# Kernel tuning notes

Hardware: AMD Instinct MI355X
Metric: run time of the kernel (lower is better)

The kernel has to match this reference:

```python
import jax, jax.numpy as jnp
import numpy as np

D_MODEL = 1024
H = 16
D_K = D_MODEL // H

def setup_inputs() -> dict:
    key = jax.random.key(0)
    k1, k2, k3, k4, k5 = jax.random.split(key, 5)
    x = jax.random.normal(k1, (2, 2048, D_MODEL), dtype=jnp.float32)
    s = 1.0 / np.sqrt(D_MODEL)
    W_qkv = jax.random.uniform(k2, (D_MODEL, 3 * D_MODEL), jnp.float32, -s, s)
    b_qkv = jax.random.uniform(k3, (3 * D_MODEL,), jnp.float32, -s, s)
    W_o = jax.random.uniform(k4, (D_MODEL, D_MODEL), jnp.float32, -s, s)
    b_o = jax.random.uniform(k5, (D_MODEL,), jnp.float32, -s, s)
    return {"x": x, "W_qkv": W_qkv, "b_qkv": b_qkv, "W_o": W_o, "b_o": b_o}

def reference(x, W_qkv, b_qkv, W_o, b_o):
    B, L, _ = x.shape
    qkv = x @ W_qkv + b_qkv                      # [B, L, 3*d_model]
    q, k, v = jnp.split(qkv, 3, axis=-1)
    def split_heads(t):
        return t.reshape(B, L, H, D_K).transpose(0, 2, 1, 3)  # [B,H,L,D_k]
    q, k, v = split_heads(q), split_heads(k), split_heads(v)
    scores = jnp.einsum('bhqd,bhkd->bhqk', q, k) / np.sqrt(D_K).astype(jnp.float32)
    attn = jax.nn.softmax(scores, axis=-1)       # [B,H,L,L]
    ctx = jnp.einsum('bhqk,bhkd->bhqd', attn, v)
    ctx = ctx.transpose(0, 2, 1, 3).reshape(B, L, H * D_K)
    out = ctx @ W_o + b_o                        # dropout is identity at eval
    return (out, attn)
```

## Files before the change

kernel.cpp:

```cpp
#include <hip/hip_runtime.h>
#include <stdint.h>

typedef __attribute__((ext_vector_type(8))) short bf16x8;
typedef __attribute__((ext_vector_type(4))) float f32x4;
typedef __attribute__((ext_vector_type(4))) unsigned int u32x4;
typedef __attribute__((ext_vector_type(4))) unsigned short u16x4;

#define DEVINL static __device__ __forceinline__

DEVINL unsigned short f2bf(float f) {
  uint32_t u = __builtin_bit_cast(uint32_t, f);
  u = (u + 0x7FFFu + ((u >> 16) & 1u)) >> 16;
  return (unsigned short)u;
}

DEVINL float fexp2(float x) {
#if __has_builtin(__builtin_amdgcn_exp2f)
  return __builtin_amdgcn_exp2f(x);
#else
  return __expf(x * 0.69314718056f);
#endif
}

DEVINL void raw_barrier() {
  __builtin_amdgcn_sched_barrier(0);
  __builtin_amdgcn_s_barrier();
  __builtin_amdgcn_sched_barrier(0);
}

DEVINL void barrier_lds_only() {
  asm volatile("s_waitcnt lgkmcnt(0)" ::: "memory");
  raw_barrier();
}

DEVINL bf16x8 pack8(f32x4 a, f32x4 b) {
  union { uint32_t u[4]; bf16x8 v; } r;
  asm("v_cvt_pk_bf16_f32 %0, %1, %2" : "=v"(r.u[0]) : "v"(a[0]), "v"(a[1]));
  asm("v_cvt_pk_bf16_f32 %0, %1, %2" : "=v"(r.u[1]) : "v"(a[2]), "v"(a[3]));
  asm("v_cvt_pk_bf16_f32 %0, %1, %2" : "=v"(r.u[2]) : "v"(b[0]), "v"(b[1]));
  asm("v_cvt_pk_bf16_f32 %0, %1, %2" : "=v"(r.u[3]) : "v"(b[2]), "v"(b[3]));
  return r.v;
}

DEVINL void async16(const unsigned short* lds, const unsigned short* g) {
  __builtin_amdgcn_global_load_lds(
      (const __attribute__((address_space(1))) unsigned int*)g,
      (__attribute__((address_space(3))) unsigned int*)lds, 16, 0, 0);
}

__global__ __launch_bounds__(256) void k_prep(const float* __restrict__ x,
                                              unsigned short* __restrict__ xbf,
                                              const float* __restrict__ Wqkv,
                                              unsigned short* __restrict__ wqT,
                                              const float* __restrict__ Wo,
                                              unsigned short* __restrict__ woT) {
  int bid = blockIdx.x;
  int t = threadIdx.x;
  if (bid < 4096) {
    int i = bid * 256 + t;
    f32x4 v = *(const f32x4*)(x + (size_t)i * 4);
    u16x4 o;
    for (int j = 0; j < 4; ++j) o[j] = f2bf(v[j]);
    *(u16x4*)(xbf + (size_t)i * 4) = o;
    return;
  }
  __shared__ unsigned short tile[64][72];
  const float* in;
  unsigned short* out;
  int K = 1024, N, k0, n0;
  if (bid < 4864) {
    int b = bid - 4096;
    N = 3072; k0 = (b & 15) * 64; n0 = (b >> 4) * 64;
    in = Wqkv; out = wqT;
  } else {
    int b = bid - 4864;
    N = 1024; k0 = (b & 15) * 64; n0 = (b >> 4) * 64;
    in = Wo; out = woT;
  }
  int r = t >> 2, c0 = (t & 3) * 16;
  for (int j = 0; j < 4; ++j) {
    int col = c0 + j * 4;
    f32x4 v = *(const f32x4*)(in + (size_t)(k0 + r) * N + n0 + col);
    u16x4 o;
    for (int q = 0; q < 4; ++q) o[q] = f2bf(v[q]);
    *(u16x4*)(&tile[r][col]) = o;
  }
  __syncthreads();
  for (int j = 0; j < 4; ++j) {
    int kcol = c0 + j * 4;
    u16x4 o;
    for (int q = 0; q < 4; ++q) o[q] = tile[kcol + q][r];
    *(u16x4*)(out + (size_t)(n0 + r) * K + k0 + kcol) = o;
  }
}

template <int MODE>
__global__ __launch_bounds__(256) void k_gemm(const unsigned short* __restrict__ A,
                                              const unsigned short* __restrict__ Bt,
                                              const float* __restrict__ bias,
                                              unsigned short* __restrict__ Qb,
                                              unsigned short* __restrict__ Kb,
                                              unsigned short* __restrict__ Vt,
                                              float* __restrict__ outF) {
  constexpr int KD = 1024;
  __shared__ unsigned short sh[17408];
  unsigned short* lA = sh;
  unsigned short* lB = sh + 8192;
  int tid = threadIdx.x;
  int lane = tid & 63, w = tid >> 6;
  int wr = w >> 1, wc = w & 1;
  int m0 = blockIdx.x * 128, n0 = blockIdx.y * 128;
  int lr = lane & 15, lg = lane >> 4;

  f32x4 acc[4][4] = {};

  int srow = w * 32 + (lane >> 3);
  int scol = (lane & 7) * 8;
  const unsigned short* gA = A + (size_t)(m0 + srow) * KD + scol;
  const unsigned short* gB = Bt + (size_t)(n0 + srow) * KD + scol;

  for (int kk = 0; kk < KD; kk += 64) {
    for (int s = 0; s < 4; ++s) {
      async16(&lA[(w * 32 + s * 8) * 64], gA + (size_t)s * 8 * KD + kk);
      async16(&lB[(w * 32 + s * 8) * 64], gB + (size_t)s * 8 * KD + kk);
    }
    __syncthreads();
    for (int kq = 0; kq < 2; ++kq) {
      bf16x8 af[4], bfr[4];
      for (int i = 0; i < 4; ++i)
        af[i] = *(const bf16x8*)(&lA[(wr * 64 + i * 16 + lr) * 64 + (kq * 4 + lg) * 8]);
      for (int r = 0; r < 4; ++r)
        bfr[r] = *(const bf16x8*)(&lB[(wc * 64 + r * 16 + lr) * 64 + (kq * 4 + lg) * 8]);
      for (int i = 0; i < 4; ++i)
        for (int r = 0; r < 4; ++r)
          acc[i][r] = __builtin_amdgcn_mfma_f32_16x16x32_bf16(af[i], bfr[r], acc[i][r], 0, 0, 0);
    }
    __syncthreads();
  }

  if (MODE == 0) {
    int which = n0 >> 10;
    int head0 = (n0 & 1023) >> 6;
    int b_idx = m0 >> 11;
    int l0 = m0 & 2047;
    if (which < 2) {
      for (int r = 0; r < 4; ++r) {
        int nl = wc * 64 + r * 16 + lr;
        float bv = bias[n0 + nl];
        for (int i = 0; i < 4; ++i) {
          int mlb = wr * 64 + i * 16 + lg * 4;
          for (int jj = 0; jj < 4; ++jj)
            sh[(mlb + jj) * 136 + nl] = f2bf(acc[i][r][jj] + bv);
        }
      }
      __syncthreads();
      unsigned short* dst = (which == 0) ? Qb : Kb;
      for (int it = 0; it < 4; ++it) {
        int row = it * 64 + (tid >> 2);
        int ml = row & 127, hd = row >> 7;
        int c = (tid & 3) * 16;
        bf16x8 v0 = *(const bf16x8*)&sh[ml * 136 + hd * 64 + c];
        bf16x8 v1 = *(const bf16x8*)&sh[ml * 136 + hd * 64 + c + 8];
        size_t bh = (size_t)(b_idx * 16 + head0 + hd);
        size_t off = (bh * 2048 + l0 + ml) * 64 + c;
        *(bf16x8*)(dst + off) = v0;
        *(bf16x8*)(dst + off + 8) = v1;
      }
    } else {
      for (int r = 0; r < 4; ++r) {
        int nl = wc * 64 + r * 16 + lr;
        float bv = bias[n0 + nl];
        for (int i = 0; i < 4; ++i) {
          int mlb = wr * 64 + i * 16 + lg * 4;
          u16x4 pk;
          for (int jj = 0; jj < 4; ++jj) pk[jj] = f2bf(acc[i][r][jj] + bv);
          *(u16x4*)&sh[nl * 136 + mlb] = pk;
        }
      }
      __syncthreads();
      for (int it = 0; it < 4; ++it) {
        int nl = it * 32 + (tid >> 3);
        int c = (tid & 7) * 16;
        bf16x8 v0 = *(const bf16x8*)&sh[nl * 136 + c];
        bf16x8 v1 = *(const bf16x8*)&sh[nl * 136 + c + 8];
        int dk = nl & 63, hd = nl >> 6;
        size_t bh = (size_t)(b_idx * 16 + head0 + hd);
        size_t off = (bh * 64 + dk) * 2048 + l0 + c;
        *(bf16x8*)(Vt + off) = v0;
        *(bf16x8*)(Vt + off + 8) = v1;
      }
    }
  } else {
    for (int r = 0; r < 4; ++r) {
      int n = n0 + wc * 64 + r * 16 + lr;
      float bv = bias[n];
      for (int i = 0; i < 4; ++i) {
        int mb = m0 + wr * 64 + i * 16 + lg * 4;
        for (int jj = 0; jj < 4; ++jj)
          outF[(size_t)(mb + jj) * 1024 + n] = acc[i][r][jj] + bv;
      }
    }
  }
}

__global__ __launch_bounds__(256) void k_attn(const unsigned short* __restrict__ Qb,
                                              const unsigned short* __restrict__ Kb,
                                              const unsigned short* __restrict__ Vt,
                                              float* __restrict__ attn,
                                              unsigned short* __restrict__ ctx) {
  __shared__ unsigned short Ks[2][4096];
  __shared__ unsigned short Vs[2][4096];
  __shared__ float Pf[4][32 * 68];
  int tid = threadIdx.x, lane = tid & 63, w = tid >> 6;
  int lr = lane & 15, lg = lane >> 4;
  int bid = blockIdx.x;
  int xcd = bid & 7, slot = bid >> 3;
  int bh = xcd * 4 + (slot >> 4);
  int qb = slot & 15;
  int q0 = qb * 128 + w * 32;
  int b_idx = bh >> 4, h = bh & 15;
  const unsigned short* Qh = Qb + (size_t)bh * 2048 * 64;
  const unsigned short* Kh = Kb + (size_t)bh * 2048 * 64;
  const unsigned short* Vh = Vt + (size_t)bh * 64 * 2048;
  float* Pw = &Pf[w][0];
  const float A2 = 0.125f * 1.44269504089f;
  int e7 = lr & 7;

  int srow = w * 8 + (lane >> 3);
  int sc = (lane & 7) ^ (srow & 7);
  const unsigned short* gK = Kh + (size_t)srow * 64 + sc * 8;
  const unsigned short* gV = Vh + (size_t)srow * 2048 + sc * 8;

  bf16x8 qf[2][2];
  for (int i = 0; i < 2; ++i)
    for (int kq = 0; kq < 2; ++kq)
      qf[i][kq] = *(const bf16x8*)(Qh + (size_t)(q0 + i * 16 + lr) * 64 + kq * 32 + lg * 8);

  float l_run[2] = {0.f, 0.f};

  async16(&Ks[0][(w * 8) * 64],       gK);
  async16(&Ks[0][((w + 4) * 8) * 64], gK + 2048);
  for (int kt = 0; kt < 32; ++kt) {
    int cur = kt & 1;
    if (kt < 31) {
      async16(&Ks[cur ^ 1][(w * 8) * 64],       gK + (size_t)(kt + 1) * 4096);
      async16(&Ks[cur ^ 1][((w + 4) * 8) * 64], gK + (size_t)(kt + 1) * 4096 + 2048);
      asm volatile("s_waitcnt vmcnt(2)" ::: "memory");
    } else {
      asm volatile("s_waitcnt vmcnt(0)" ::: "memory");
    }
    raw_barrier();
    f32x4 acc[2][4] = {};
    for (int kq = 0; kq < 2; ++kq) {
      int j = kq * 4 + lg;
      bf16x8 kf[4];
      for (int r = 0; r < 4; ++r)
        kf[r] = *(const bf16x8*)&Ks[cur][(r * 16 + lr) * 64 + ((j ^ e7) << 3)];
      for (int i = 0; i < 2; ++i)
        for (int r = 0; r < 4; ++r)
          acc[i][r] = __builtin_amdgcn_mfma_f32_16x16x32_bf16(kf[r], qf[i][kq], acc[i][r], 0, 0, 0);
    }
    for (int i = 0; i < 2; ++i)
      for (int r = 0; r < 4; ++r)
        l_run[i] += fexp2(acc[i][r][0] * A2) + fexp2(acc[i][r][1] * A2) +
                    fexp2(acc[i][r][2] * A2) + fexp2(acc[i][r][3] * A2);
    barrier_lds_only();
  }
  float invl[2];
  for (int i = 0; i < 2; ++i) {
    float s = l_run[i];
    s += __shfl_xor(s, 16);
    s += __shfl_xor(s, 32);
    invl[i] = 1.0f / s;
  }

  f32x4 cacc[2][4] = {};
  float* attn_base = attn + (size_t)bh * 2048 * 2048;
  float* arow = attn_base + (size_t)(q0 + lg) * 2048 + lr * 4;

  async16(&Ks[0][(w * 8) * 64],       gK);
  async16(&Ks[0][((w + 4) * 8) * 64], gK + 2048);
  async16(&Vs[0][(w * 8) * 64],       gV);
  async16(&Vs[0][((w + 4) * 8) * 64], gV + 65536);
  for (int kt = 0; kt < 32; ++kt) {
    int cur = kt & 1;
    if (kt < 31) {
      async16(&Ks[cur ^ 1][(w * 8) * 64],       gK + (size_t)(kt + 1) * 4096);
      async16(&Ks[cur ^ 1][((w + 4) * 8) * 64], gK + (size_t)(kt + 1) * 4096 + 2048);
      async16(&Vs[cur ^ 1][(w * 8) * 64],       gV + (size_t)(kt + 1) * 64);
      async16(&Vs[cur ^ 1][((w + 4) * 8) * 64], gV + (size_t)(kt + 1) * 64 + 65536);
    }
    if (kt == 0)       asm volatile("s_waitcnt vmcnt(4)" ::: "memory");
    else if (kt == 31) asm volatile("s_waitcnt vmcnt(8)" ::: "memory");
    else               asm volatile("s_waitcnt vmcnt(12)" ::: "memory");
    raw_barrier();
    f32x4 acc[2][4] = {};
    for (int kq = 0; kq < 2; ++kq) {
      int j = kq * 4 + lg;
      bf16x8 kf[4];
      for (int r = 0; r < 4; ++r)
        kf[r] = *(const bf16x8*)&Ks[cur][(r * 16 + lr) * 64 + ((j ^ e7) << 3)];
      for (int i = 0; i < 2; ++i)
        for (int r = 0; r < 4; ++r)
          acc[i][r] = __builtin_amdgcn_mfma_f32_16x16x32_bf16(kf[r], qf[i][kq], acc[i][r], 0, 0, 0);
    }
    for (int i = 0; i < 2; ++i)
      for (int r = 0; r < 4; ++r) {
        f32x4 pv;
        for (int jj = 0; jj < 4; ++jj)
          pv[jj] = fexp2(acc[i][r][jj] * A2) * invl[i];
        *(f32x4*)&Pw[(i * 16 + lr) * 68 + r * 16 + lg * 4] = pv;
      }
    for (int s = 0; s < 8; ++s) {
      f32x4 v = *(const f32x4*)(&Pw[(s * 4 + lg) * 68 + lr * 4]);
      __builtin_nontemporal_store(v, (f32x4*)(arow + (size_t)s * 4 * 2048 + kt * 64));
    }
    for (int kq2 = 0; kq2 < 2; ++kq2) {
      int j = kq2 * 4 + lg;
      int kof = kq2 * 32 + lg * 8;
      bf16x8 pa[2], vf[4];
      for (int i = 0; i < 2; ++i) {
        f32x4 plo = *(const f32x4*)(&Pw[(i * 16 + lr) * 68 + kof]);
        f32x4 phi = *(const f32x4*)(&Pw[(i * 16 + lr) * 68 + kof + 4]);
        pa[i] = pack8(plo, phi);
      }
      for (int nn = 0; nn < 4; ++nn)
        vf[nn] = *(const bf16x8*)&Vs[cur][(nn * 16 + lr) * 64 + ((j ^ e7) << 3)];
      for (int i = 0; i < 2; ++i)
        for (int nn = 0; nn < 4; ++nn)
          cacc[i][nn] = __builtin_amdgcn_mfma_f32_16x16x32_bf16(pa[i], vf[nn], cacc[i][nn], 0, 0, 0);
    }
    barrier_lds_only();
  }

  for (int nn = 0; nn < 4; ++nn) {
    int d = nn * 16 + lr;
    for (int i = 0; i < 2; ++i)
      for (int jj = 0; jj < 4; ++jj) {
        int q = q0 + i * 16 + lg * 4 + jj;
        int tok = b_idx * 2048 + q;
        ctx[(size_t)tok * 1024 + h * 64 + d] = f2bf(cacc[i][nn][jj]);
      }
  }
}

extern "C" void kernel_launch(void* const* d_in, const int* in_sizes, int n_in,
                              void* d_out, int out_size, void* d_ws, size_t ws_size,
                              hipStream_t stream) {
  const float* x    = (const float*)d_in[0];
  const float* Wqkv = (const float*)d_in[1];
  const float* bqkv = (const float*)d_in[2];
  const float* Wo   = (const float*)d_in[3];
  const float* bo   = (const float*)d_in[4];
  float* out  = (float*)d_out;
  float* attn = out + (size_t)4096 * 1024;

  char* ws = (char*)d_ws;
  unsigned short* xbf = (unsigned short*)(ws);
  unsigned short* wqT = (unsigned short*)(ws + 8388608);
  unsigned short* woT = (unsigned short*)(ws + 14680064);
  unsigned short* Qb  = (unsigned short*)(ws + 16777216);
  unsigned short* Kb  = (unsigned short*)(ws + 25165824);
  unsigned short* Vt  = (unsigned short*)(ws + 33554432);
  unsigned short* ctx = (unsigned short*)(ws + 41943040);

  k_prep<<<dim3(5120), dim3(256), 0, stream>>>(x, xbf, Wqkv, wqT, Wo, woT);
  k_gemm<0><<<dim3(32, 24), dim3(256), 0, stream>>>(xbf, wqT, bqkv, Qb, Kb, Vt, nullptr);
  k_attn<<<dim3(512), dim3(256), 0, stream>>>(Qb, Kb, Vt, attn, ctx);
  k_gemm<1><<<dim3(32, 8), dim3(256), 0, stream>>>(ctx, woT, bo, nullptr, nullptr, nullptr, out);
}
```

Measured before the change: 232.9 us.

## Stage softmax probabilities as bf16 in LDS and deepen K prefetch ring

The attention kernel now converts probabilities to packed bf16 once and keeps them in a bf16 LDS buffer. That buffer feeds the PV MFMA directly and is widened back to fp32 for the attn output store, which halves the P staging footprint and removes the fp32 re-read and repack. K and V buffers are merged into one 4-slot LDS array. The first (row-sum) pass uses a prefetch distance of two with the per-iteration trailing barrier removed. The returned attention matrix is now rounded to bf16 precision, which adds output error, and the lower LDS use may allow higher occupancy.

```diff
diff --git a/kernel.cpp b/kernel.cpp
--- a/kernel.cpp
+++ b/kernel.cpp
@@ -4,6 +4,7 @@
 typedef __attribute__((ext_vector_type(8))) short bf16x8;
 typedef __attribute__((ext_vector_type(4))) float f32x4;
 typedef __attribute__((ext_vector_type(4))) unsigned int u32x4;
+typedef __attribute__((ext_vector_type(2))) unsigned int u32x2;
 typedef __attribute__((ext_vector_type(4))) unsigned short u16x4;
 
 #define DEVINL static __device__ __forceinline__
@@ -31,15 +32,6 @@
 DEVINL void barrier_lds_only() {
   asm volatile("s_waitcnt lgkmcnt(0)" ::: "memory");
   raw_barrier();
-}
-
-DEVINL bf16x8 pack8(f32x4 a, f32x4 b) {
-  union { uint32_t u[4]; bf16x8 v; } r;
-  asm("v_cvt_pk_bf16_f32 %0, %1, %2" : "=v"(r.u[0]) : "v"(a[0]), "v"(a[1]));
-  asm("v_cvt_pk_bf16_f32 %0, %1, %2" : "=v"(r.u[1]) : "v"(a[2]), "v"(a[3]));
-  asm("v_cvt_pk_bf16_f32 %0, %1, %2" : "=v"(r.u[2]) : "v"(b[0]), "v"(b[1]));
-  asm("v_cvt_pk_bf16_f32 %0, %1, %2" : "=v"(r.u[3]) : "v"(b[2]), "v"(b[3]));
-  return r.v;
 }
 
 DEVINL void async16(const unsigned short* lds, const unsigned short* g) {
@@ -208,9 +200,8 @@
                                               const unsigned short* __restrict__ Vt,
                                               float* __restrict__ attn,
                                               unsigned short* __restrict__ ctx) {
-  __shared__ unsigned short Ks[2][4096];
-  __shared__ unsigned short Vs[2][4096];
-  __shared__ float Pf[4][32 * 68];
+  __shared__ unsigned short KVs[4][4096];
+  __shared__ uint32_t Pb[4][32 * 36];
   int tid = threadIdx.x, lane = tid & 63, w = tid >> 6;
   int lr = lane & 15, lg = lane >> 4;
   int bid = blockIdx.x;
@@ -222,7 +213,7 @@
   const unsigned short* Qh = Qb + (size_t)bh * 2048 * 64;
   const unsigned short* Kh = Kb + (size_t)bh * 2048 * 64;
   const unsigned short* Vh = Vt + (size_t)bh * 64 * 2048;
-  float* Pw = &Pf[w][0];
+  uint32_t* PwB = &Pb[w][0];
   const float A2 = 0.125f * 1.44269504089f;
   int e7 = lr & 7;
 
@@ -238,13 +229,17 @@
 
   float l_run[2] = {0.f, 0.f};
 
-  async16(&Ks[0][(w * 8) * 64],       gK);
-  async16(&Ks[0][((w + 4) * 8) * 64], gK + 2048);
+  async16(&KVs[0][(w * 8) * 64],       gK);
+  async16(&KVs[0][((w + 4) * 8) * 64], gK + 2048);
+  async16(&KVs[1][(w * 8) * 64],       gK + 4096);
+  async16(&KVs[1][((w + 4) * 8) * 64], gK + 4096 + 2048);
   for (int kt = 0; kt < 32; ++kt) {
-    int cur = kt & 1;
-    if (kt < 31) {
-      async16(&Ks[cur ^ 1][(w * 8) * 64],       gK + (size_t)(kt + 1) * 4096);
-      async16(&Ks[cur ^ 1][((w + 4) * 8) * 64], gK + (size_t)(kt + 1) * 4096 + 2048);
+    const unsigned short* Kc = KVs[kt & 3];
+    if (kt < 30) {
+      async16(&KVs[(kt + 2) & 3][(w * 8) * 64],       gK + (size_t)(kt + 2) * 4096);
+      async16(&KVs[(kt + 2) & 3][((w + 4) * 8) * 64], gK + (size_t)(kt + 2) * 4096 + 2048);
+      asm volatile("s_waitcnt vmcnt(4)" ::: "memory");
+    } else if (kt == 30) {
       asm volatile("s_waitcnt vmcnt(2)" ::: "memory");
     } else {
       asm volatile("s_waitcnt vmcnt(0)" ::: "memory");
@@ -255,7 +250,7 @@
       int j = kq * 4 + lg;
       bf16x8 kf[4];
       for (int r = 0; r < 4; ++r)
-        kf[r] = *(const bf16x8*)&Ks[cur][(r * 16 + lr) * 64 + ((j ^ e7) << 3)];
+        kf[r] = *(const bf16x8*)&Kc[(r * 16 + lr) * 64 + ((j ^ e7) << 3)];
       for (int i = 0; i < 2; ++i)
         for (int r = 0; r < 4; ++r)
           acc[i][r] = __builtin_amdgcn_mfma_f32_16x16x32_bf16(kf[r], qf[i][kq], acc[i][r], 0, 0, 0);
@@ -264,7 +259,6 @@
       for (int r = 0; r < 4; ++r)
         l_run[i] += fexp2(acc[i][r][0] * A2) + fexp2(acc[i][r][1] * A2) +
                     fexp2(acc[i][r][2] * A2) + fexp2(acc[i][r][3] * A2);
-    barrier_lds_only();
   }
   float invl[2];
   for (int i = 0; i < 2; ++i) {
@@ -278,54 +272,64 @@
   float* attn_base = attn + (size_t)bh * 2048 * 2048;
   float* arow = attn_base + (size_t)(q0 + lg) * 2048 + lr * 4;
 
-  async16(&Ks[0][(w * 8) * 64],       gK);
-  async16(&Ks[0][((w + 4) * 8) * 64], gK + 2048);
-  async16(&Vs[0][(w * 8) * 64],       gV);
-  async16(&Vs[0][((w + 4) * 8) * 64], gV + 65536);
+  barrier_lds_only();
+  async16(&KVs[0][(w * 8) * 64],       gK);
+  async16(&KVs[0][((w + 4) * 8) * 64], gK + 2048);
+  async16(&KVs[2][(w * 8) * 64],       gV);
+  async16(&KVs[2][((w + 4) * 8) * 64], gV + 65536);
   for (int kt = 0; kt < 32; ++kt) {
     int cur = kt & 1;
     if (kt < 31) {
-      async16(&Ks[cur ^ 1][(w * 8) * 64],       gK + (size_t)(kt + 1) * 4096);
-      async16(&Ks[cur ^ 1][((w + 4) * 8) * 64], gK + (size_t)(kt + 1) * 4096 + 2048);
-      async16(&Vs[cur ^ 1][(w * 8) * 64],       gV + (size_t)(kt + 1) * 64);
-      async16(&Vs[cur ^ 1][((w + 4) * 8) * 64], gV + (size_t)(kt + 1) * 64 + 65536);
+      async16(&KVs[cur ^ 1][(w * 8) * 64],       gK + (size_t)(kt + 1) * 4096);
+      async16(&KVs[cur ^ 1][((w + 4) * 8) * 64], gK + (size_t)(kt + 1) * 4096 + 2048);
+      async16(&KVs[2 + (cur ^ 1)][(w * 8) * 64],       gV + (size_t)(kt + 1) * 64);
+      async16(&KVs[2 + (cur ^ 1)][((w + 4) * 8) * 64], gV + (size_t)(kt + 1) * 64 + 65536);
     }
     if (kt == 0)       asm volatile("s_waitcnt vmcnt(4)" ::: "memory");
     else if (kt == 31) asm volatile("s_waitcnt vmcnt(8)" ::: "memory");
     else               asm volatile("s_waitcnt vmcnt(12)" ::: "memory");
     raw_barrier();
+    const unsigned short* Kc = KVs[cur];
+    const unsigned short* Vc = KVs[2 + cur];
     f32x4 acc[2][4] = {};
     for (int kq = 0; kq < 2; ++kq) {
       int j = kq * 4 + lg;
       bf16x8 kf[4];
       for (int r = 0; r < 4; ++r)
-        kf[r] = *(const bf16x8*)&Ks[cur][(r * 16 + lr) * 64 + ((j ^ e7) << 3)];
+        kf[r] = *(const bf16x8*)&Kc[(r * 16 + lr) * 64 + ((j ^ e7) << 3)];
       for (int i = 0; i < 2; ++i)
         for (int r = 0; r < 4; ++r)
           acc[i][r] = __builtin_amdgcn_mfma_f32_16x16x32_bf16(kf[r], qf[i][kq], acc[i][r], 0, 0, 0);
     }
     for (int i = 0; i < 2; ++i)
       for (int r = 0; r < 4; ++r) {
-        f32x4 pv;
-        for (int jj = 0; jj < 4; ++jj)
-          pv[jj] = fexp2(acc[i][r][jj] * A2) * invl[i];
-        *(f32x4*)&Pw[(i * 16 + lr) * 68 + r * 16 + lg * 4] = pv;
+        float p0 = fexp2(acc[i][r][0] * A2) * invl[i];
+        float p1 = fexp2(acc[i][r][1] * A2) * invl[i];
+        float p2 = fexp2(acc[i][r][2] * A2) * invl[i];
+        float p3 = fexp2(acc[i][r][3] * A2) * invl[i];
+        uint32_t u0, u1;
+        asm("v_cvt_pk_bf16_f32 %0, %1, %2" : "=v"(u0) : "v"(p0), "v"(p1));
+        asm("v_cvt_pk_bf16_f32 %0, %1, %2" : "=v"(u1) : "v"(p2), "v"(p3));
+        u32x2 uu; uu[0] = u0; uu[1] = u1;
+        *(u32x2*)&PwB[(i * 16 + lr) * 36 + r * 8 + lg * 2] = uu;
       }
     for (int s = 0; s < 8; ++s) {
-      f32x4 v = *(const f32x4*)(&Pw[(s * 4 + lg) * 68 + lr * 4]);
+      int row = s * 4 + lg;
+      u32x2 d = *(const u32x2*)&PwB[row * 36 + lr * 2];
+      f32x4 v;
+      v[0] = __builtin_bit_cast(float, d[0] << 16);
+      v[1] = __builtin_bit_cast(float, d[0] & 0xFFFF0000u);
+      v[2] = __builtin_bit_cast(float, d[1] << 16);
+      v[3] = __builtin_bit_cast(float, d[1] & 0xFFFF0000u);
       __builtin_nontemporal_store(v, (f32x4*)(arow + (size_t)s * 4 * 2048 + kt * 64));
     }
     for (int kq2 = 0; kq2 < 2; ++kq2) {
       int j = kq2 * 4 + lg;
-      int kof = kq2 * 32 + lg * 8;
       bf16x8 pa[2], vf[4];
-      for (int i = 0; i < 2; ++i) {
-        f32x4 plo = *(const f32x4*)(&Pw[(i * 16 + lr) * 68 + kof]);
-        f32x4 phi = *(const f32x4*)(&Pw[(i * 16 + lr) * 68 + kof + 4]);
-        pa[i] = pack8(plo, phi);
-      }
+      for (int i = 0; i < 2; ++i)
+        pa[i] = *(const bf16x8*)&PwB[(i * 16 + lr) * 36 + kq2 * 16 + lg * 4];
       for (int nn = 0; nn < 4; ++nn)
-        vf[nn] = *(const bf16x8*)&Vs[cur][(nn * 16 + lr) * 64 + ((j ^ e7) << 3)];
+        vf[nn] = *(const bf16x8*)&Vc[(nn * 16 + lr) * 64 + ((j ^ e7) << 3)];
       for (int i = 0; i < 2; ++i)
         for (int nn = 0; nn < 4; ++nn)
           cacc[i][nn] = __builtin_amdgcn_mfma_f32_16x16x32_bf16(pa[i], vf[nn], cacc[i][nn], 0, 0, 0);
```

New measurement: 222.7 us. 1.05x faster.
